# Kernel tuning notes

Measured on AMD Instinct MI355X. Metric: run time of the kernel, lower is better.

Reference implementation:

```python
import jax, jax.numpy as jnp
import numpy as np

N_MEM = 500_000
D_LATENT = 512
D_QUERY = 768


def setup_inputs() -> dict:
    key = jax.random.key(0)
    ks = jax.random.split(key, 8)
    s = 1.0 / np.sqrt(D_QUERY)
    s2 = 1.0 / np.sqrt(2 * D_LATENT)
    s3 = 1.0 / np.sqrt(D_LATENT)
    return {
        "query": jax.random.normal(ks[0], (D_QUERY,), dtype=jnp.float32),
        "memory": jax.random.normal(ks[1], (N_MEM, D_LATENT), dtype=jnp.float32),
        "Wp": jax.random.uniform(ks[2], (D_LATENT, D_QUERY), jnp.float32, -s, s),
        "bp": jax.random.uniform(ks[3], (D_LATENT,), jnp.float32, -s, s),
        "W1": jax.random.uniform(ks[4], (D_LATENT, 2 * D_LATENT), jnp.float32, -s2, s2),
        "b1": jax.random.uniform(ks[5], (D_LATENT,), jnp.float32, -s2, s2),
        "W2": jax.random.uniform(ks[6], (1, D_LATENT), jnp.float32, -s3, s3),
        "b2": jax.random.uniform(ks[7], (1,), jnp.float32, -s3, s3),
        "k": 16,
    }


def reference(query, memory, Wp, bp, W1, b1, W2, b2, k):
    # query projection: [d_query] -> [d_latent]
    q = Wp @ query + bp  # [D_LATENT]
    # memory bank retrieve: cosine similarity, top 2k candidates
    qn = q / (jnp.linalg.norm(q) + 1e-8)
    mn = memory / (jnp.linalg.norm(memory, axis=-1, keepdims=True) + 1e-8)
    sims = mn @ qn  # [N_MEM]
    _, cand_idx = jax.lax.top_k(sims, 2 * k)  # [2k]
    cand = memory[cand_idx]  # [2k, D_LATENT]
    # batched rerank MLP: concat(query_latent, candidate) -> Linear -> ReLU -> Linear
    combined = jnp.concatenate(
        [jnp.broadcast_to(q, (2 * k, D_LATENT)), cand], axis=-1
    )  # [2k, 2*D_LATENT]
    h = jax.nn.relu(combined @ W1.T + b1)  # [2k, D_LATENT]
    scores = (h @ W2.T + b2)[:, 0]  # [2k]
    # sort by rerank score (desc), keep top k
    top_scores, sel = jax.lax.top_k(scores, k)
    return top_scores, cand_idx[sel]
```

## Files before the change

kernel.cpp:

```cpp
#include <hip/hip_runtime.h>
#include <hip/hip_bf16.h>
#include <math.h>

static constexpr size_t SIMS_OFF   = 0;
static constexpr size_t Q_OFF      = 500736;
static constexpr size_t QN_OFF     = 501248;
static constexpr size_t HIST_OFF   = 501760;
static constexpr size_t COUNT_OFF  = 505856;
static constexpr size_t THRESH_OFF = 505872;
static constexpr size_t CANDV_OFF  = 505888;
static constexpr size_t CANDI_OFF  = 514080;
static constexpr size_t SELI_OFF   = 522272;
static constexpr size_t SELV_OFF   = 522304;
static constexpr size_t COMB_OFF   = 522336;
static constexpr size_t H_OFF      = 555104;

static constexpr int D_LAT   = 512;
static constexpr int D_QRY   = 768;
static constexpr int NBUCKET = 4096;
static constexpr int CAND_CAP= 8192;
static constexpr int K2      = 32;
static constexpr int K1      = 16;

__global__ __launch_bounds__(512) void k_proj(
    const float* __restrict__ Wp, const float* __restrict__ query,
    const float* __restrict__ bp, float* __restrict__ q, float* __restrict__ qn) {
  const int tid  = threadIdx.x;
  const int lane = tid & 63;
  const int wave = tid >> 6;
  __shared__ float s_q[D_LAT];
  __shared__ float s_red[512];

  const float4* q4 = (const float4*)query;
  float4 qq0 = q4[lane*3+0], qq1 = q4[lane*3+1], qq2 = q4[lane*3+2];

  for (int i = wave; i < D_LAT; i += 8) {
    const float4* w4 = (const float4*)(Wp + (size_t)i * D_QRY);
    float4 w0 = w4[lane*3+0], w1 = w4[lane*3+1], w2 = w4[lane*3+2];
    float acc = w0.x*qq0.x + w0.y*qq0.y + w0.z*qq0.z + w0.w*qq0.w
              + w1.x*qq1.x + w1.y*qq1.y + w1.z*qq1.z + w1.w*qq1.w
              + w2.x*qq2.x + w2.y*qq2.y + w2.z*qq2.z + w2.w*qq2.w;
#pragma unroll
    for (int off = 32; off; off >>= 1) acc += __shfl_xor(acc, off, 64);
    if (lane == 0) {
      float v = acc + bp[i];
      s_q[i] = v;
      q[i]   = v;
    }
  }
  __syncthreads();

  float v = s_q[tid];
  s_red[tid] = v * v;
  __syncthreads();
  for (int s = 256; s > 0; s >>= 1) {
    if (tid < s) s_red[tid] += s_red[tid + s];
    __syncthreads();
  }
  float nrm = sqrtf(s_red[0]) + 1e-8f;
  qn[tid] = v / nrm;
}

__global__ __launch_bounds__(256) void k_sims(
    const float* __restrict__ mem, const float* __restrict__ qn,
    float* __restrict__ sims, unsigned* __restrict__ ghist, int nrows) {
  __shared__ unsigned hist[NBUCKET];
  for (int i = threadIdx.x; i < NBUCKET; i += 256) hist[i] = 0;
  __syncthreads();

  const int lane   = threadIdx.x & 63;
  const int wave   = (blockIdx.x * 256 + threadIdx.x) >> 6;
  const int nwaves = (gridDim.x * 256) >> 6;

  const float4* qn4 = (const float4*)qn;
  float4 qa = qn4[lane*2], qb = qn4[lane*2+1];

  for (int row = wave; row < nrows; row += nwaves) {
    const float4* m4 = (const float4*)(mem + (size_t)row * D_LAT);
    float4 a = m4[lane*2], b = m4[lane*2+1];
    float dot = a.x*qa.x + a.y*qa.y + a.z*qa.z + a.w*qa.w
              + b.x*qb.x + b.y*qb.y + b.z*qb.z + b.w*qb.w;
    float ss  = a.x*a.x + a.y*a.y + a.z*a.z + a.w*a.w
              + b.x*b.x + b.y*b.y + b.z*b.z + b.w*b.w;
#pragma unroll
    for (int off = 32; off; off >>= 1) {
      dot += __shfl_xor(dot, off, 64);
      ss  += __shfl_xor(ss,  off, 64);
    }
    if (lane == 0) {
      float s = dot / (sqrtf(ss) + 1e-8f);
      sims[row] = s;
      int bkt = (int)((s + 1.0f) * 2048.0f);
      bkt = bkt < 0 ? 0 : (bkt > NBUCKET-1 ? NBUCKET-1 : bkt);
      atomicAdd(&hist[bkt], 1u);
    }
  }
  __syncthreads();
  for (int i = threadIdx.x; i < NBUCKET; i += 256)
    if (hist[i]) atomicAdd(&ghist[i], hist[i]);
}

__global__ void k_thresh(const unsigned* __restrict__ ghist, float* __restrict__ thresh) {
  if (threadIdx.x == 0 && blockIdx.x == 0) {
    unsigned c = 0; int b = NBUCKET - 1;
    for (; b >= 0; --b) { c += ghist[b]; if (c >= (unsigned)K2) break; }
    if (b < 0) b = 0;
    thresh[0] = (float)b * (1.0f/2048.0f) - 1.0f - 1e-6f;
  }
}

__global__ __launch_bounds__(256) void k_collect(
    const float* __restrict__ sims, const float* __restrict__ thresh,
    float* __restrict__ cv, int* __restrict__ ci, unsigned* __restrict__ count, int n) {
  float t = thresh[0];
  int stride = gridDim.x * 256;
  for (int i = blockIdx.x * 256 + threadIdx.x; i < n; i += stride) {
    float v = sims[i];
    if (v >= t) {
      unsigned p = atomicAdd(count, 1u);
      if (p < (unsigned)CAND_CAP) { cv[p] = v; ci[p] = i; }
    }
  }
}

__global__ __launch_bounds__(256) void k_select(
    const float* __restrict__ cv, const int* __restrict__ ci,
    const unsigned* __restrict__ count, const float* __restrict__ q,
    const float* __restrict__ mem, int* __restrict__ seli,
    float* __restrict__ selv, float* __restrict__ comb) {
  __shared__ int   s_idx[K2];
  __shared__ float s_val[K2];
  if (threadIdx.x == 0) {
    int n = (int)(*count);
    if (n > CAND_CAP) n = CAND_CAP;
    float pv = 1e30f; int pi = -1;
    for (int s = 0; s < K2; ++s) {
      float bv = -1e30f; int bi = 0x7fffffff;
      for (int j = 0; j < n; ++j) {
        float v = cv[j]; int id = ci[j];
        if (v > pv || (v == pv && id <= pi)) continue;
        if (v > bv || (v == bv && id < bi)) { bv = v; bi = id; }
      }
      s_val[s] = bv; s_idx[s] = bi;
      pv = bv; pi = bi;
    }
  }
  __syncthreads();
  if (threadIdx.x < K2) { seli[threadIdx.x] = s_idx[threadIdx.x]; selv[threadIdx.x] = s_val[threadIdx.x]; }
  for (int t = threadIdx.x; t < K2 * 2 * D_LAT; t += 256) {
    int c = t >> 10, j = t & 1023;
    comb[t] = (j < D_LAT) ? q[j] : mem[(size_t)s_idx[c] * D_LAT + (j - D_LAT)];
  }
}

__global__ __launch_bounds__(256) void k_mlp1(
    const float* __restrict__ comb, const float* __restrict__ W1,
    const float* __restrict__ b1, float* __restrict__ h) {
  int t = blockIdx.x * 256 + threadIdx.x;
  int c = t & 31, i = t >> 5;
  const float4* w4 = (const float4*)(W1 + (size_t)i * (2*D_LAT));
  const float4* c4 = (const float4*)(comb + (size_t)c * (2*D_LAT));
  float acc = 0.f;
#pragma unroll 8
  for (int j = 0; j < (2*D_LAT)/4; ++j) {
    float4 w = w4[j], x = c4[j];
    acc += w.x*x.x + w.y*x.y + w.z*x.z + w.w*x.w;
  }
  acc += b1[i];
  h[(size_t)c * D_LAT + i] = fmaxf(acc, 0.f);
}

__global__ __launch_bounds__(64) void k_final(
    const float* __restrict__ h, const float* __restrict__ W2,
    const float* __restrict__ b2, const int* __restrict__ seli,
    float* __restrict__ out) {
  __shared__ float sc[K2];
  if (threadIdx.x < K2) {
    const float* hr = h + (size_t)threadIdx.x * D_LAT;
    float acc = 0.f;
    for (int i = 0; i < D_LAT; ++i) acc += hr[i] * W2[i];
    sc[threadIdx.x] = acc + b2[0];
  }
  __syncthreads();
  if (threadIdx.x == 0) {
    float pv = 1e30f; int pc = -1;
    for (int s = 0; s < K1; ++s) {
      float bv = -1e30f; int bc = 0;
      for (int c = 0; c < K2; ++c) {
        float v = sc[c];
        if (v > pv || (v == pv && c <= pc)) continue;
        if (v > bv) { bv = v; bc = c; }
      }
      out[s]      = bv;
      out[K1 + s] = (float)seli[bc];
      pv = bv; pc = bc;
    }
  }
}

extern "C" void kernel_launch(void* const* d_in, const int* in_sizes, int n_in,
                              void* d_out, int out_size, void* d_ws, size_t ws_size,
                              hipStream_t stream) {
  (void)n_in; (void)out_size; (void)ws_size;
  const float* query  = (const float*)d_in[0];
  const float* memory = (const float*)d_in[1];
  const float* Wp     = (const float*)d_in[2];
  const float* bp     = (const float*)d_in[3];
  const float* W1     = (const float*)d_in[4];
  const float* b1     = (const float*)d_in[5];
  const float* W2     = (const float*)d_in[6];
  const float* b2     = (const float*)d_in[7];
  const int nrows = in_sizes[1] / D_LAT;

  float*    ws    = (float*)d_ws;
  float*    sims  = ws + SIMS_OFF;
  float*    q     = ws + Q_OFF;
  float*    qn    = ws + QN_OFF;
  unsigned* hist  = (unsigned*)(ws + HIST_OFF);
  unsigned* count = (unsigned*)(ws + COUNT_OFF);
  float*    thr   = ws + THRESH_OFF;
  float*    candv = ws + CANDV_OFF;
  int*      candi = (int*)(ws + CANDI_OFF);
  int*      seli  = (int*)(ws + SELI_OFF);
  float*    selv  = ws + SELV_OFF;
  float*    comb  = ws + COMB_OFF;
  float*    h     = ws + H_OFF;
  float*    out   = (float*)d_out;

  hipMemsetAsync(hist, 0, (NBUCKET + 16) * sizeof(unsigned), stream);
  k_proj   <<<1,    512, 0, stream>>>(Wp, query, bp, q, qn);
  k_sims   <<<4096, 256, 0, stream>>>(memory, qn, sims, hist, nrows);
  k_thresh <<<1,     64, 0, stream>>>(hist, thr);
  k_collect<<<256,  256, 0, stream>>>(sims, thr, candv, candi, count, nrows);
  k_select <<<1,    256, 0, stream>>>(candv, candi, count, q, memory, seli, selv, comb);
  k_mlp1   <<<64,   256, 0, stream>>>(comb, W1, b1, h);
  k_final  <<<1,     64, 0, stream>>>(h, W2, b2, seli, out);
}
```

Before: 1.681 ms.

## Parallelize query projection across blocks and top-k selection via rank counting

The query projection moves from a single 512-thread block to 128 blocks with one wave per row, and the L2 norm moves into a separate small kernel. The single-threaded repeated-scan top-32 selection becomes a parallel rank computation: candidates are packed into sortable 64-bit keys in shared memory and each thread counts how many keys exceed its own. This removes serial bottlenecks at the cost of an extra kernel launch and O(n^2) comparisons that grow with candidate count.

```diff
diff --git a/kernel.cpp b/kernel.cpp
--- a/kernel.cpp
+++ b/kernel.cpp
@@ -22,35 +22,30 @@
 static constexpr int K2      = 32;
 static constexpr int K1      = 16;
 
-__global__ __launch_bounds__(512) void k_proj(
+__global__ __launch_bounds__(256) void k_proj_dot(
     const float* __restrict__ Wp, const float* __restrict__ query,
-    const float* __restrict__ bp, float* __restrict__ q, float* __restrict__ qn) {
-  const int tid  = threadIdx.x;
-  const int lane = tid & 63;
-  const int wave = tid >> 6;
-  __shared__ float s_q[D_LAT];
-  __shared__ float s_red[512];
+    const float* __restrict__ bp, float* __restrict__ q) {
+  const int lane = threadIdx.x & 63;
+  const int row  = (blockIdx.x * 256 + threadIdx.x) >> 6;
 
   const float4* q4 = (const float4*)query;
   float4 qq0 = q4[lane*3+0], qq1 = q4[lane*3+1], qq2 = q4[lane*3+2];
 
-  for (int i = wave; i < D_LAT; i += 8) {
-    const float4* w4 = (const float4*)(Wp + (size_t)i * D_QRY);
-    float4 w0 = w4[lane*3+0], w1 = w4[lane*3+1], w2 = w4[lane*3+2];
-    float acc = w0.x*qq0.x + w0.y*qq0.y + w0.z*qq0.z + w0.w*qq0.w
-              + w1.x*qq1.x + w1.y*qq1.y + w1.z*qq1.z + w1.w*qq1.w
-              + w2.x*qq2.x + w2.y*qq2.y + w2.z*qq2.z + w2.w*qq2.w;
+  const float4* w4 = (const float4*)(Wp + (size_t)row * D_QRY);
+  float4 w0 = w4[lane*3+0], w1 = w4[lane*3+1], w2 = w4[lane*3+2];
+  float acc = w0.x*qq0.x + w0.y*qq0.y + w0.z*qq0.z + w0.w*qq0.w
+            + w1.x*qq1.x + w1.y*qq1.y + w1.z*qq1.z + w1.w*qq1.w
+            + w2.x*qq2.x + w2.y*qq2.y + w2.z*qq2.z + w2.w*qq2.w;
 #pragma unroll
-    for (int off = 32; off; off >>= 1) acc += __shfl_xor(acc, off, 64);
-    if (lane == 0) {
-      float v = acc + bp[i];
-      s_q[i] = v;
-      q[i]   = v;
-    }
-  }
-  __syncthreads();
-
-  float v = s_q[tid];
+  for (int off = 32; off; off >>= 1) acc += __shfl_xor(acc, off, 64);
+  if (lane == 0) q[row] = acc + bp[row];
+}
+
+__global__ __launch_bounds__(512) void k_norm(
+    const float* __restrict__ q, float* __restrict__ qn) {
+  __shared__ float s_red[512];
+  const int tid = threadIdx.x;
+  float v = q[tid];
   s_red[tid] = v * v;
   __syncthreads();
   for (int s = 256; s > 0; s >>= 1) {
@@ -123,31 +118,36 @@
   }
 }
 
-__global__ __launch_bounds__(256) void k_select(
+__global__ __launch_bounds__(1024) void k_select(
     const float* __restrict__ cv, const int* __restrict__ ci,
     const unsigned* __restrict__ count, const float* __restrict__ q,
     const float* __restrict__ mem, int* __restrict__ seli,
-    float* __restrict__ selv, float* __restrict__ comb) {
-  __shared__ int   s_idx[K2];
-  __shared__ float s_val[K2];
-  if (threadIdx.x == 0) {
-    int n = (int)(*count);
-    if (n > CAND_CAP) n = CAND_CAP;
-    float pv = 1e30f; int pi = -1;
-    for (int s = 0; s < K2; ++s) {
-      float bv = -1e30f; int bi = 0x7fffffff;
-      for (int j = 0; j < n; ++j) {
-        float v = cv[j]; int id = ci[j];
-        if (v > pv || (v == pv && id <= pi)) continue;
-        if (v > bv || (v == bv && id < bi)) { bv = v; bi = id; }
-      }
-      s_val[s] = bv; s_idx[s] = bi;
-      pv = bv; pi = bi;
-    }
-  }
-  __syncthreads();
-  if (threadIdx.x < K2) { seli[threadIdx.x] = s_idx[threadIdx.x]; selv[threadIdx.x] = s_val[threadIdx.x]; }
-  for (int t = threadIdx.x; t < K2 * 2 * D_LAT; t += 256) {
+    float* __restrict__ comb) {
+  __shared__ unsigned long long keys[CAND_CAP];
+  __shared__ int s_idx[K2];
+  const int tid = threadIdx.x;
+  if (tid < K2) s_idx[tid] = 0;
+
+  int n = (int)(*count);
+  if (n > CAND_CAP) n = CAND_CAP;
+
+  for (int j = tid; j < n; j += 1024) {
+    unsigned u = __float_as_uint(cv[j]);
+    u = (u & 0x80000000u) ? ~u : (u | 0x80000000u);
+    keys[j] = ((unsigned long long)u << 32)
+            | (unsigned long long)(0xFFFFFFFFu - (unsigned)ci[j]);
+  }
+  __syncthreads();
+
+  for (int j = tid; j < n; j += 1024) {
+    unsigned long long k = keys[j];
+    int r = 0;
+    for (int i = 0; i < n; ++i) r += (keys[i] > k) ? 1 : 0;
+    if (r < K2) { s_idx[r] = ci[j]; seli[r] = ci[j]; }
+  }
+  __syncthreads();
+
+  for (int t = tid; t < K2 * 2 * D_LAT; t += 1024) {
     int c = t >> 10, j = t & 1023;
     comb[t] = (j < D_LAT) ? q[j] : mem[(size_t)s_idx[c] * D_LAT + (j - D_LAT)];
   }
@@ -222,17 +222,17 @@
   float*    candv = ws + CANDV_OFF;
   int*      candi = (int*)(ws + CANDI_OFF);
   int*      seli  = (int*)(ws + SELI_OFF);
-  float*    selv  = ws + SELV_OFF;
   float*    comb  = ws + COMB_OFF;
   float*    h     = ws + H_OFF;
   float*    out   = (float*)d_out;
 
   hipMemsetAsync(hist, 0, (NBUCKET + 16) * sizeof(unsigned), stream);
-  k_proj   <<<1,    512, 0, stream>>>(Wp, query, bp, q, qn);
-  k_sims   <<<4096, 256, 0, stream>>>(memory, qn, sims, hist, nrows);
-  k_thresh <<<1,     64, 0, stream>>>(hist, thr);
-  k_collect<<<256,  256, 0, stream>>>(sims, thr, candv, candi, count, nrows);
-  k_select <<<1,    256, 0, stream>>>(candv, candi, count, q, memory, seli, selv, comb);
-  k_mlp1   <<<64,   256, 0, stream>>>(comb, W1, b1, h);
-  k_final  <<<1,     64, 0, stream>>>(h, W2, b2, seli, out);
-}
+  k_proj_dot<<<128,  256, 0, stream>>>(Wp, query, bp, q);
+  k_norm    <<<1,    512, 0, stream>>>(q, qn);
+  k_sims    <<<4096, 256, 0, stream>>>(memory, qn, sims, hist, nrows);
+  k_thresh  <<<1,     64, 0, stream>>>(hist, thr);
+  k_collect <<<256,  256, 0, stream>>>(sims, thr, candv, candi, count, nrows);
+  k_select  <<<1,   1024, 0, stream>>>(candv, candi, count, q, memory, seli, comb);
+  k_mlp1    <<<64,   256, 0, stream>>>(comb, W1, b1, h);
+  k_final   <<<1,     64, 0, stream>>>(h, W2, b2, seli, out);
+}
```

Measured after the change: 1.482 ms. 1.13x faster.
